# Optimization experiments

Hardware: AMD Instinct MI355X
Metric: run time of the kernel (lower is better)

The kernel has to match this reference:

```python
import jax, jax.numpy as jnp
import numpy as np

N_IN = 1024
LAYER_SIZES = [2048] * 8 + [1024]  # 8 hidden layers + output layer
DEG = 32
BATCH = 1024


def setup_inputs() -> dict:
    key = jax.random.key(0)
    kx, kw, ki = jax.random.split(key, 3)
    X = jax.random.normal(kx, (BATCH, N_IN), dtype=jnp.float32)
    weight = jnp.float32(0.5)  # net.best_w, shared scalar across all nodes
    # Topologically valid children: nodes in layer l may reference any
    # previously computed node (index < offset).
    idx_blocks = []
    offset = N_IN
    for li, sz in enumerate(LAYER_SIZES):
        k = jax.random.fold_in(ki, li)
        idx_blocks.append(jax.random.randint(k, (sz, DEG), 0, offset, dtype=jnp.int32))
        offset += sz
    child_idx = jnp.concatenate(idx_blocks, axis=0)  # [sum(LAYER_SIZES), DEG]
    return {"X": X, "weight": weight, "child_idx": child_idx}


def reference(X, weight, child_idx):
    # X: [B, N_IN]; child_idx: [n_compute_nodes, DEG] (topologically ordered)
    # Each node: val = tanh(weight * sum(child_vals))  (params = w*ones(deg))
    vals = X  # input-layer node values, [B, n_nodes_so_far]
    ptr = 0
    for sz in LAYER_SIZES:
        idx = child_idx[ptr:ptr + sz]          # [sz, DEG], static slice
        ptr += sz
        gathered = vals[:, idx]                # [B, sz, DEG]
        new = jnp.tanh(weight * gathered.sum(axis=-1))  # [B, sz]
        vals = jnp.concatenate([vals, new], axis=1)
    n_out = LAYER_SIZES[-1]
    return vals[:, -n_out:]  # [B, n_outputs]
```

## Files before the change

kernel.cpp:

```cpp
#include <hip/hip_runtime.h>

#define BATCH 1024
#define N_IN 1024
#define TOTAL 18432
#define BLOCK 1024
#define NNEUR 17408

__device__ __forceinline__ float fast_tanh(float x) {
    float e = __expf(2.0f * x);
    return 1.0f - 2.0f / (1.0f + e);
}

#define PREP_T 256
__global__ __launch_bounds__(PREP_T) void prep_kernel(const int4* __restrict__ cidx4,
                                                      int4* __restrict__ idxT) {
    __shared__ int out_s[32 * PREP_T];
    __shared__ int left_s[32 * PREP_T];
    const int m = blockIdx.x * PREP_T + threadIdx.x;
    const int tid = threadIdx.x;
    if (m >= NNEUR) return;

    const int layer = min(m >> 11, 8);
    const int nloc  = m - (layer << 11);
    const int sz    = (layer == 8) ? 1024 : 2048;
    const int ptr   = layer << 11;
    const int lane  = nloc & 63;
    const int hiFirst = (lane & 1) << 4;

    const int4* src = cidx4 + (size_t)m * 8;
    int4 v[8];
    #pragma unroll
    for (int g = 0; g < 8; ++g) v[g] = src[g];

    unsigned slotFree = 0xFFFFFFFFu;
    int nleft = 0;
    #pragma unroll
    for (int g = 0; g < 8; ++g) {
        int comp[4] = {v[g].x, v[g].y, v[g].z, v[g].w};
        #pragma unroll
        for (int c = 0; c < 4; ++c) {
            const int id = comp[c];
            const int s1 = ((id & 15) - lane) & 15;
            const int sA = s1 + hiFirst;
            const int sB = s1 + (hiFirst ^ 16);
            if (slotFree >> sA & 1u) {
                out_s[sA * PREP_T + tid] = id;
                slotFree &= ~(1u << sA);
            } else if (slotFree >> sB & 1u) {
                out_s[sB * PREP_T + tid] = id;
                slotFree &= ~(1u << sB);
            } else {
                left_s[nleft * PREP_T + tid] = id;
                ++nleft;
            }
        }
    }
    unsigned f = slotFree;
    for (int i = 0; i < nleft; ++i) {
        const int s = __builtin_ctz(f);
        f &= f - 1;
        out_s[s * PREP_T + tid] = left_s[i * PREP_T + tid];
    }
    int4* dst = idxT + (size_t)ptr * 8;
    #pragma unroll
    for (int g = 0; g < 8; ++g) {
        int4 o;
        o.x = out_s[(4 * g + 0) * PREP_T + tid];
        o.y = out_s[(4 * g + 1) * PREP_T + tid];
        o.z = out_s[(4 * g + 2) * PREP_T + tid];
        o.w = out_s[(4 * g + 3) * PREP_T + tid];
        dst[(size_t)g * sz + nloc] = o;
    }
}

__global__ __launch_bounds__(BLOCK) void net_kernel_t(
    const float* __restrict__ X,
    const float* __restrict__ wptr,
    const int4* __restrict__ idxT,
    float* __restrict__ out)
{
    __shared__ float2 vals[TOTAL];
    const int rowA = blockIdx.x * 2;
    const float w = wptr[0];
    const int t = threadIdx.x;

    {
        const float4* xa = reinterpret_cast<const float4*>(X + (size_t)rowA * N_IN);
        const float4* xb = reinterpret_cast<const float4*>(X + (size_t)(rowA + 1) * N_IN);
        for (int i = t; i < N_IN / 4; i += BLOCK) {
            float4 a = xa[i], b = xb[i];
            vals[4 * i + 0] = make_float2(a.x, b.x);
            vals[4 * i + 1] = make_float2(a.y, b.y);
            vals[4 * i + 2] = make_float2(a.z, b.z);
            vals[4 * i + 3] = make_float2(a.w, b.w);
        }
    }
    __syncthreads();

    int off = N_IN;
    const int4* L = idxT;
    #pragma unroll
    for (int li = 0; li < 9; ++li) {
        const int sz = (li == 8) ? 1024 : 2048;
        if (sz == 2048) {
            const int n0 = t, n1 = t + 1024;
            float a0x = 0.f, a0y = 0.f, a1x = 0.f, a1y = 0.f;
            #pragma unroll
            for (int g = 0; g < 8; ++g) {
                int4 i0 = L[(size_t)g * 2048 + n0];
                int4 i1 = L[(size_t)g * 2048 + n1];
                float2 p = vals[i0.x], q = vals[i0.y], u = vals[i0.z], s = vals[i0.w];
                a0x += (p.x + q.x) + (u.x + s.x);
                a0y += (p.y + q.y) + (u.y + s.y);
                p = vals[i1.x]; q = vals[i1.y]; u = vals[i1.z]; s = vals[i1.w];
                a1x += (p.x + q.x) + (u.x + s.x);
                a1y += (p.y + q.y) + (u.y + s.y);
            }
            vals[off + n0] = make_float2(fast_tanh(w * a0x), fast_tanh(w * a0y));
            vals[off + n1] = make_float2(fast_tanh(w * a1x), fast_tanh(w * a1y));
        } else {
            const int n0 = t;
            float a0x = 0.f, a0y = 0.f;
            #pragma unroll
            for (int g = 0; g < 8; ++g) {
                int4 i0 = L[(size_t)g * 1024 + n0];
                float2 p = vals[i0.x], q = vals[i0.y], u = vals[i0.z], s = vals[i0.w];
                a0x += (p.x + q.x) + (u.x + s.x);
                a0y += (p.y + q.y) + (u.y + s.y);
            }
            vals[off + n0] = make_float2(fast_tanh(w * a0x), fast_tanh(w * a0y));
        }
        __syncthreads();
        off += sz;
        L += (size_t)sz * 8;
    }

    {
        float* oA = out + (size_t)rowA * 1024;
        float* oB = out + (size_t)(rowA + 1) * 1024;
        const float2* src = vals + (TOTAL - 1024);
        for (int i = t; i < 1024; i += BLOCK) {
            float2 v = src[i];
            oA[i] = v.x;
            oB[i] = v.y;
        }
    }
}

__global__ __launch_bounds__(BLOCK) void net_kernel_f(
    const float* __restrict__ X,
    const float* __restrict__ wptr,
    const int* __restrict__ cidx,
    float* __restrict__ out)
{
    __shared__ float2 vals[TOTAL];
    const int rowA = blockIdx.x * 2;
    const float w = wptr[0];
    const int t = threadIdx.x;
    {
        const float4* xa = reinterpret_cast<const float4*>(X + (size_t)rowA * N_IN);
        const float4* xb = reinterpret_cast<const float4*>(X + (size_t)(rowA + 1) * N_IN);
        for (int i = t; i < N_IN / 4; i += BLOCK) {
            float4 a = xa[i], b = xb[i];
            vals[4 * i + 0] = make_float2(a.x, b.x);
            vals[4 * i + 1] = make_float2(a.y, b.y);
            vals[4 * i + 2] = make_float2(a.z, b.z);
            vals[4 * i + 3] = make_float2(a.w, b.w);
        }
    }
    __syncthreads();
    int off = N_IN, ptr = 0;
    #pragma unroll
    for (int li = 0; li < 9; ++li) {
        const int sz = (li == 8) ? 1024 : 2048;
        for (int n = t; n < sz; n += BLOCK) {
            const int4* ip = reinterpret_cast<const int4*>(cidx + (size_t)(ptr + n) * 32);
            float sx = 0.f, sy = 0.f;
            #pragma unroll
            for (int j = 0; j < 8; ++j) {
                const int4 v = ip[j];
                float2 a = vals[v.x], b = vals[v.y], c = vals[v.z], d = vals[v.w];
                sx += (a.x + b.x) + (c.x + d.x);
                sy += (a.y + b.y) + (c.y + d.y);
            }
            vals[off + n] = make_float2(fast_tanh(w * sx), fast_tanh(w * sy));
        }
        __syncthreads();
        off += sz;
        ptr += sz;
    }
    {
        float* oA = out + (size_t)rowA * 1024;
        float* oB = out + (size_t)(rowA + 1) * 1024;
        const float2* src = vals + (TOTAL - 1024);
        for (int i = t; i < 1024; i += BLOCK) {
            float2 v = src[i];
            oA[i] = v.x;
            oB[i] = v.y;
        }
    }
}

extern "C" void kernel_launch(void* const* d_in, const int* in_sizes, int n_in,
                              void* d_out, int out_size, void* d_ws, size_t ws_size,
                              hipStream_t stream)
{
    const float* X    = (const float*)d_in[0];
    const float* w    = (const float*)d_in[1];
    const int*   cidx = (const int*)d_in[2];
    float* out = (float*)d_out;

    const size_t need = (size_t)NNEUR * 32 * sizeof(int);
    if (ws_size >= need) {
        int4* idxT = (int4*)d_ws;
        hipLaunchKernelGGL(prep_kernel, dim3((NNEUR + PREP_T - 1) / PREP_T), dim3(PREP_T), 0, stream,
                           (const int4*)cidx, idxT);
        hipLaunchKernelGGL(net_kernel_t, dim3(BATCH / 2), dim3(BLOCK), 0, stream,
                           X, w, idxT, out);
    } else {
        hipLaunchKernelGGL(net_kernel_f, dim3(BATCH / 2), dim3(BLOCK), 0, stream,
                           X, w, cidx, out);
    }
}
```

Measured before the change: 126.0 us.

## Balance LDS bank usage in index prep and write final layer directly to output

The prep kernel now runs one 64-thread wavefront per block and keeps shared per-slot bank counters. Leftover child indices go to the free slot with the fewest same-bank entries instead of the first free slot, which should cut LDS bank conflicts in the gather. The main kernel shrinks its shared value array by not storing the final layer and writes that layer's tanh results straight to global memory. This adds atomics and extra barriers to the prep kernel, and the smaller final-layer writes may coalesce less well.

```diff
diff --git a/kernel.cpp b/kernel.cpp
--- a/kernel.cpp
+++ b/kernel.cpp
@@ -3,35 +3,39 @@
 #define BATCH 1024
 #define N_IN 1024
 #define TOTAL 18432
+#define VTOT  17408
 #define BLOCK 1024
 #define NNEUR 17408
+#define NUNITS 272
 
 __device__ __forceinline__ float fast_tanh(float x) {
     float e = __expf(2.0f * x);
     return 1.0f - 2.0f / (1.0f + e);
 }
 
-#define PREP_T 256
-__global__ __launch_bounds__(PREP_T) void prep_kernel(const int4* __restrict__ cidx4,
-                                                      int4* __restrict__ idxT) {
-    __shared__ int out_s[32 * PREP_T];
-    __shared__ int left_s[32 * PREP_T];
-    const int m = blockIdx.x * PREP_T + threadIdx.x;
-    const int tid = threadIdx.x;
-    if (m >= NNEUR) return;
-
-    const int layer = min(m >> 11, 8);
-    const int nloc  = m - (layer << 11);
+__global__ __launch_bounds__(64) void prep_kernel(const int4* __restrict__ cidx4,
+                                                  int4* __restrict__ idxT) {
+    __shared__ int out_s[32 * 64];
+    __shared__ int left_s[32 * 64];
+    __shared__ int cnt[32 * 16];
+    const int lane = threadIdx.x;
+    const int b = blockIdx.x;
+    const int layer = (b < 256) ? (b >> 5) : 8;
+    const int group = (b < 256) ? (b & 31) : (b - 256);
     const int sz    = (layer == 8) ? 1024 : 2048;
     const int ptr   = layer << 11;
-    const int lane  = nloc & 63;
-    const int hiFirst = (lane & 1) << 4;
+    const int nloc  = group * 64 + lane;
+    const int m     = ptr + nloc;
+
+    for (int i = lane; i < 32 * 16; i += 64) cnt[i] = 0;
 
     const int4* src = cidx4 + (size_t)m * 8;
     int4 v[8];
     #pragma unroll
     for (int g = 0; g < 8; ++g) v[g] = src[g];
-
+    __syncthreads();
+
+    const int hiFirst = (lane & 1) << 4;
     unsigned slotFree = 0xFFFFFFFFu;
     int nleft = 0;
     #pragma unroll
@@ -40,35 +44,56 @@
         #pragma unroll
         for (int c = 0; c < 4; ++c) {
             const int id = comp[c];
-            const int s1 = ((id & 15) - lane) & 15;
+            const int r  = id & 15;
+            const int s1 = (r - lane) & 15;
             const int sA = s1 + hiFirst;
             const int sB = s1 + (hiFirst ^ 16);
             if (slotFree >> sA & 1u) {
-                out_s[sA * PREP_T + tid] = id;
+                out_s[sA * 64 + lane] = id;
                 slotFree &= ~(1u << sA);
+                atomicAdd(&cnt[sA * 16 + r], 1);
             } else if (slotFree >> sB & 1u) {
-                out_s[sB * PREP_T + tid] = id;
+                out_s[sB * 64 + lane] = id;
                 slotFree &= ~(1u << sB);
+                atomicAdd(&cnt[sB * 16 + r], 1);
             } else {
-                left_s[nleft * PREP_T + tid] = id;
+                left_s[nleft * 64 + lane] = id;
                 ++nleft;
             }
         }
     }
-    unsigned f = slotFree;
-    for (int i = 0; i < nleft; ++i) {
-        const int s = __builtin_ctz(f);
-        f &= f - 1;
-        out_s[s * PREP_T + tid] = left_s[i * PREP_T + tid];
-    }
+    __syncthreads();
+
+    for (int i = 0; i < 32; ++i) {
+        unsigned long long act = __ballot(i < nleft);
+        if (act == 0ull) break;
+        if (i < nleft) {
+            const int id = left_s[i * 64 + lane];
+            const int r  = id & 15;
+            unsigned f = slotFree;
+            int bestS = -1, bestC = 1 << 30;
+            while (f) {
+                const int s = __builtin_ctz(f);
+                f &= f - 1;
+                const int c = cnt[s * 16 + r];
+                if (c < bestC) { bestC = c; bestS = s; }
+            }
+            atomicAdd(&cnt[bestS * 16 + r], 1);
+            out_s[bestS * 64 + lane] = id;
+            slotFree &= ~(1u << bestS);
+        }
+        __syncthreads();
+    }
+    __syncthreads();
+
     int4* dst = idxT + (size_t)ptr * 8;
     #pragma unroll
     for (int g = 0; g < 8; ++g) {
         int4 o;
-        o.x = out_s[(4 * g + 0) * PREP_T + tid];
-        o.y = out_s[(4 * g + 1) * PREP_T + tid];
-        o.z = out_s[(4 * g + 2) * PREP_T + tid];
-        o.w = out_s[(4 * g + 3) * PREP_T + tid];
+        o.x = out_s[(4 * g + 0) * 64 + lane];
+        o.y = out_s[(4 * g + 1) * 64 + lane];
+        o.z = out_s[(4 * g + 2) * 64 + lane];
+        o.w = out_s[(4 * g + 3) * 64 + lane];
         dst[(size_t)g * sz + nloc] = o;
     }
 }
@@ -79,7 +104,7 @@
     const int4* __restrict__ idxT,
     float* __restrict__ out)
 {
-    __shared__ float2 vals[TOTAL];
+    __shared__ float2 vals[VTOT];
     const int rowA = blockIdx.x * 2;
     const float w = wptr[0];
     const int t = threadIdx.x;
@@ -100,50 +125,39 @@
     int off = N_IN;
     const int4* L = idxT;
     #pragma unroll
-    for (int li = 0; li < 9; ++li) {
-        const int sz = (li == 8) ? 1024 : 2048;
-        if (sz == 2048) {
-            const int n0 = t, n1 = t + 1024;
-            float a0x = 0.f, a0y = 0.f, a1x = 0.f, a1y = 0.f;
-            #pragma unroll
-            for (int g = 0; g < 8; ++g) {
-                int4 i0 = L[(size_t)g * 2048 + n0];
-                int4 i1 = L[(size_t)g * 2048 + n1];
-                float2 p = vals[i0.x], q = vals[i0.y], u = vals[i0.z], s = vals[i0.w];
-                a0x += (p.x + q.x) + (u.x + s.x);
-                a0y += (p.y + q.y) + (u.y + s.y);
-                p = vals[i1.x]; q = vals[i1.y]; u = vals[i1.z]; s = vals[i1.w];
-                a1x += (p.x + q.x) + (u.x + s.x);
-                a1y += (p.y + q.y) + (u.y + s.y);
-            }
-            vals[off + n0] = make_float2(fast_tanh(w * a0x), fast_tanh(w * a0y));
-            vals[off + n1] = make_float2(fast_tanh(w * a1x), fast_tanh(w * a1y));
-        } else {
-            const int n0 = t;
-            float a0x = 0.f, a0y = 0.f;
-            #pragma unroll
-            for (int g = 0; g < 8; ++g) {
-                int4 i0 = L[(size_t)g * 1024 + n0];
-                float2 p = vals[i0.x], q = vals[i0.y], u = vals[i0.z], s = vals[i0.w];
-                a0x += (p.x + q.x) + (u.x + s.x);
-                a0y += (p.y + q.y) + (u.y + s.y);
-            }
-            vals[off + n0] = make_float2(fast_tanh(w * a0x), fast_tanh(w * a0y));
-        }
+    for (int li = 0; li < 8; ++li) {
+        const int n0 = t, n1 = t + 1024;
+        float a0x = 0.f, a0y = 0.f, a1x = 0.f, a1y = 0.f;
+        #pragma unroll
+        for (int g = 0; g < 8; ++g) {
+            int4 i0 = L[(size_t)g * 2048 + n0];
+            int4 i1 = L[(size_t)g * 2048 + n1];
+            float2 p = vals[i0.x], q = vals[i0.y], u = vals[i0.z], s = vals[i0.w];
+            a0x += (p.x + q.x) + (u.x + s.x);
+            a0y += (p.y + q.y) + (u.y + s.y);
+            p = vals[i1.x]; q = vals[i1.y]; u = vals[i1.z]; s = vals[i1.w];
+            a1x += (p.x + q.x) + (u.x + s.x);
+            a1y += (p.y + q.y) + (u.y + s.y);
+        }
+        vals[off + n0] = make_float2(fast_tanh(w * a0x), fast_tanh(w * a0y));
+        vals[off + n1] = make_float2(fast_tanh(w * a1x), fast_tanh(w * a1y));
         __syncthreads();
-        off += sz;
-        L += (size_t)sz * 8;
-    }
-
-    {
-        float* oA = out + (size_t)rowA * 1024;
-        float* oB = out + (size_t)(rowA + 1) * 1024;
-        const float2* src = vals + (TOTAL - 1024);
-        for (int i = t; i < 1024; i += BLOCK) {
-            float2 v = src[i];
-            oA[i] = v.x;
-            oB[i] = v.y;
-        }
+        off += 2048;
+        L += (size_t)2048 * 8;
+    }
+
+    {
+        const int n0 = t;
+        float a0x = 0.f, a0y = 0.f;
+        #pragma unroll
+        for (int g = 0; g < 8; ++g) {
+            int4 i0 = L[(size_t)g * 1024 + n0];
+            float2 p = vals[i0.x], q = vals[i0.y], u = vals[i0.z], s = vals[i0.w];
+            a0x += (p.x + q.x) + (u.x + s.x);
+            a0y += (p.y + q.y) + (u.y + s.y);
+        }
+        out[(size_t)rowA * 1024 + n0]       = fast_tanh(w * a0x);
+        out[(size_t)(rowA + 1) * 1024 + n0] = fast_tanh(w * a0y);
     }
 }
 
@@ -213,7 +227,7 @@
     const size_t need = (size_t)NNEUR * 32 * sizeof(int);
     if (ws_size >= need) {
         int4* idxT = (int4*)d_ws;
-        hipLaunchKernelGGL(prep_kernel, dim3((NNEUR + PREP_T - 1) / PREP_T), dim3(PREP_T), 0, stream,
+        hipLaunchKernelGGL(prep_kernel, dim3(NUNITS), dim3(64), 0, stream,
                            (const int4*)cidx, idxT);
         hipLaunchKernelGGL(net_kernel_t, dim3(BATCH / 2), dim3(BLOCK), 0, stream,
                            X, w, idxT, out);
```

After: 131.2 us. +4.2%, slower.
